# Kernel optimization log

Hardware: AMD Instinct MI355X
Metric: run time of the kernel (lower is better)

The kernel has to match this reference:

```python
import jax, jax.numpy as jnp
import numpy as np

B, S, D, H = 4, 2048, 1024, 16
HD = D // H  # 64

def setup_inputs() -> dict:
    key = jax.random.key(0)
    ks = jax.random.split(key, 6)
    scale = 1.0 / np.sqrt(D)
    return {
        "x": jax.random.normal(ks[0], (B, S, D), dtype=jnp.float32),
        "Wq": jax.random.normal(ks[1], (D, D), dtype=jnp.float32) * scale,
        "Wk": jax.random.normal(ks[2], (D, D), dtype=jnp.float32) * scale,
        "Wv": jax.random.normal(ks[3], (D, D), dtype=jnp.float32) * scale,
        "Wo": jax.random.normal(ks[4], (D, D), dtype=jnp.float32) * scale,
        "bo": jnp.zeros((D,), dtype=jnp.float32),
    }

def reference(x, Wq, Wk, Wv, Wo, bo):
    b, s, d = x.shape
    # projections (no bias for q/k/v, matching QKV_BIAS=False)
    q = (x @ Wq).reshape(b, s, H, HD).transpose(0, 2, 1, 3)  # [b,h,s,hd]
    k = (x @ Wk).reshape(b, s, H, HD).transpose(0, 2, 1, 3)
    v = (x @ Wv).reshape(b, s, H, HD).transpose(0, 2, 1, 3)
    scores = jnp.einsum('bhqd,bhkd->bhqk', q, k)  # [b,h,s,s]
    causal = jnp.tril(jnp.ones((s, s), dtype=bool))  # True where allowed
    scores = jnp.where(causal, scores, -jnp.inf)
    attn = jax.nn.softmax(scores / np.sqrt(HD), axis=-1)
    ctx = jnp.einsum('bhqk,bhkd->bhqd', attn, v)  # [b,h,s,hd]
    ctx = ctx.transpose(0, 2, 1, 3).reshape(b, s, d)
    return ctx @ Wo + bo
```

## Files before the change

kernel.cpp:

```cpp
#include <hip/hip_runtime.h>

#define BSZ 4
#define SEQ 2048
#define DIM 1024
#define NH  16
#define HD  64
#define QT  128
#define KT  64
#define PAD 72

typedef float v4f __attribute__((ext_vector_type(4)));
typedef short s8v __attribute__((ext_vector_type(8)));
typedef unsigned short u16;
typedef unsigned short u16x8 __attribute__((ext_vector_type(8)));
typedef unsigned short u16x4 __attribute__((ext_vector_type(4)));

__device__ __forceinline__ u16 f2bf(float f) {
  unsigned int u = __builtin_bit_cast(unsigned int, f);
  unsigned int r = u + 0x7fffu + ((u >> 16) & 1u);
  return (u16)(r >> 16);
}
__device__ __forceinline__ float bf2f(u16 h) {
  return __builtin_bit_cast(float, (unsigned int)h << 16);
}
__device__ __forceinline__ float fast_exp2(float x) {
#if __has_builtin(__builtin_amdgcn_exp2f)
  return __builtin_amdgcn_exp2f(x);
#else
  return exp2f(x);
#endif
}
__device__ __forceinline__ void gll16(const u16* g, u16* l) {
  __builtin_amdgcn_global_load_lds((const __attribute__((address_space(1))) void*)g,
                                   (__attribute__((address_space(3))) void*)l, 16, 0, 0);
}

__global__ __launch_bounds__(256) void cast_bf16_kernel(const float* __restrict__ x,
                                                        u16* __restrict__ o, int n4) {
  int i = blockIdx.x * 256 + threadIdx.x;
  if (i >= n4) return;
  v4f v = reinterpret_cast<const v4f*>(x)[i];
  u16x4 r;
  #pragma unroll
  for (int c = 0; c < 4; c++) r[c] = f2bf(v[c]);
  reinterpret_cast<u16x4*>(o)[i] = r;
}

__global__ __launch_bounds__(256) void transpose_cast_kernel(const float* __restrict__ W0,
                                                             const float* __restrict__ W1,
                                                             const float* __restrict__ W2,
                                                             const float* __restrict__ W3,
                                                             u16* __restrict__ out) {
  const float* W = blockIdx.z == 0 ? W0 : blockIdx.z == 1 ? W1 : blockIdx.z == 2 ? W2 : W3;
  u16* T = out + (size_t)blockIdx.z * DIM * DIM;
  __shared__ float tile[32][33];
  int tx = threadIdx.x & 31, ty = threadIdx.x >> 5;
  int bn = blockIdx.x * 32, bk = blockIdx.y * 32;
  #pragma unroll
  for (int r = 0; r < 4; r++) {
    int k = bk + ty + r * 8;
    tile[ty + r * 8][tx] = W[(size_t)k * DIM + bn + tx];
  }
  __syncthreads();
  #pragma unroll
  for (int r = 0; r < 4; r++) {
    int n = bn + ty + r * 8;
    T[(size_t)n * DIM + bk + tx] = f2bf(tile[tx][ty + r * 8]);
  }
}


#define GEMM_PROLOGUE()                                                          \
  const int t = threadIdx.x;                                                     \
  const int lane = t & 63, w = t >> 6;                                           \
  const int waveM = w >> 1, waveN = w & 1;                                       \
  const int quad = lane >> 4, l16 = lane & 15;                                   \
  __shared__ u16 Al[4096];                                                       \
  __shared__ u16 Bl[4096];                                                       \
  v4f acc[4][4];                                                                 \
  _Pragma("unroll") for (int i = 0; i < 4; i++)                                  \
    _Pragma("unroll") for (int j = 0; j < 4; j++)                                \
      acc[i][j] = (v4f){0.f, 0.f, 0.f, 0.f};                                     \
  const int sR = lane & 15, sC = lane >> 4;                                      \
  const u16* Ag0 = A  + (size_t)(m0 + (w * 2 + 0) * 16 + sR) * DIM + sC * 8;     \
  const u16* Ag1 = A  + (size_t)(m0 + (w * 2 + 1) * 16 + sR) * DIM + sC * 8;     \
  const u16* Bg0 = Bt + (size_t)(n0 + (w * 2 + 0) * 16 + sR) * DIM + sC * 8;     \
  const u16* Bg1 = Bt + (size_t)(n0 + (w * 2 + 1) * 16 + sR) * DIM + sC * 8;     \
  u16* Al0 = Al + (w * 2 + 0) * 512;                                             \
  u16* Al1 = Al + (w * 2 + 1) * 512;                                             \
  u16* Bl0 = Bl + (w * 2 + 0) * 512;                                             \
  u16* Bl1 = Bl + (w * 2 + 1) * 512;                                             \
  const int abase = waveM * 2048 + quad * 128 + l16 * 8;                         \
  const int bbase = waveN * 2048 + quad * 128 + l16 * 8;                         \
  for (int k0 = 0; k0 < DIM; k0 += 32) {                                         \
    __syncthreads();                                                             \
    gll16(Ag0 + k0, Al0); gll16(Ag1 + k0, Al1);                                  \
    gll16(Bg0 + k0, Bl0); gll16(Bg1 + k0, Bl1);                                  \
    __syncthreads();                                                             \
    s8v af[4], bfv[4];                                                           \
    _Pragma("unroll") for (int i = 0; i < 4; i++)                                \
      af[i] = *(const s8v*)(Al + abase + i * 512);                               \
    _Pragma("unroll") for (int j = 0; j < 4; j++)                                \
      bfv[j] = *(const s8v*)(Bl + bbase + j * 512);                              \
    _Pragma("unroll") for (int i = 0; i < 4; i++)                                \
      _Pragma("unroll") for (int j = 0; j < 4; j++)                              \
        acc[i][j] = __builtin_amdgcn_mfma_f32_16x16x32_bf16(af[i], bfv[j],       \
                                                            acc[i][j], 0, 0, 0); \
  }

__global__ __launch_bounds__(256) void gemm_qkv(const u16* __restrict__ A, const u16* __restrict__ Wt,
                                                u16* __restrict__ Qb, u16* __restrict__ Kb,
                                                u16* __restrict__ Vtg) {
  const int z = blockIdx.z;
  const u16* Bt = Wt + (size_t)z * DIM * DIM;
  const int n0 = blockIdx.x * 128, m0 = blockIdx.y * 128;
  GEMM_PROLOGUE()
  if (z == 2) {
    #pragma unroll
    for (int i = 0; i < 4; i++) {
      #pragma unroll
      for (int j = 0; j < 4; j++) {
        int gm0 = m0 + waveM * 64 + i * 16 + quad * 4;
        int gn = n0 + waveN * 64 + j * 16 + l16;
        int b = gm0 >> 11, s0 = gm0 & (SEQ - 1), hh = gn >> 6, d = gn & (HD - 1);
        u16x4 o;
        #pragma unroll
        for (int r = 0; r < 4; r++) o[r] = f2bf(acc[i][j][r]);
        *(u16x4*)(Vtg + ((size_t)(b * NH + hh) * HD + d) * SEQ + s0) = o;
      }
    }
  } else {
    u16* C = (z == 0) ? Qb : Kb;
    #pragma unroll
    for (int i = 0; i < 4; i++) {
      #pragma unroll
      for (int j = 0; j < 4; j++) {
        int gn = n0 + waveN * 64 + j * 16 + l16;
        #pragma unroll
        for (int r = 0; r < 4; r++) {
          int gm = m0 + waveM * 64 + i * 16 + quad * 4 + r;
          C[(size_t)gm * DIM + gn] = f2bf(acc[i][j][r]);
        }
      }
    }
  }
}

__global__ __launch_bounds__(256) void gemm_proj(const u16* __restrict__ A, const u16* __restrict__ Bt,
                                                 float* __restrict__ Cf, const float* __restrict__ bias) {
  const int n0 = blockIdx.x * 128, m0 = blockIdx.y * 128;
  GEMM_PROLOGUE()
  #pragma unroll
  for (int i = 0; i < 4; i++) {
    #pragma unroll
    for (int j = 0; j < 4; j++) {
      int gn = n0 + waveN * 64 + j * 16 + l16;
      float bv = bias[gn];
      #pragma unroll
      for (int r = 0; r < 4; r++) {
        int gm = m0 + waveM * 64 + i * 16 + quad * 4 + r;
        Cf[(size_t)gm * DIM + gn] = acc[i][j][r] + bv;
      }
    }
  }
}

__global__ __launch_bounds__(256, 2) void flash_attn_mfma(const u16* __restrict__ Qb,
                                                          const u16* __restrict__ Kb,
                                                          const u16* __restrict__ Vtg,
                                                          u16* __restrict__ Ob) {
  const int px = blockIdx.x, h = blockIdx.y, bb = blockIdx.z;
  const int t = threadIdx.x;
  const int lane = t & 63, w = t >> 6;
  const int quad = lane >> 4, l16 = lane & 15;

  __shared__ u16 QPs[QT * PAD];
  __shared__ u16 Ks[KT * PAD];
  __shared__ u16 Vs[HD * PAD];

  const size_t qkbase = (size_t)bb * SEQ * DIM + h * HD;
  const size_t vbase = ((size_t)bb * NH + h) * (size_t)HD * SEQ;

  const int vrow = t >> 2, scol = (t & 3) * 16;
  const int krow = ((vrow >> 5) + 2 * ((vrow >> 2) & 1)) * 16 + ((vrow >> 3) & 3) * 4 + (vrow & 3);

  for (int pass = 0; pass < 2; pass++) {
    const int qi = (pass == 0) ? px : (SEQ / QT - 1 - px);
    const int q0 = qi * QT;
    const int wq = q0 + w * 32;
    const int ntiles = 2 * qi + 2;

    __syncthreads();

    {
      const int r = t >> 1, c0 = (t & 1) * 32;
      const u16* src = Qb + qkbase + (size_t)(q0 + r) * DIM + c0;
      const float scq = 0.18033688011112042f;
      #pragma unroll
      for (int ch = 0; ch < 4; ch++) {
        u16x8 u = *(const u16x8*)(src + ch * 8);
        u16x8 o;
        #pragma unroll
        for (int j = 0; j < 8; j++) o[j] = f2bf(bf2f(u[j]) * scq);
        *(u16x8*)(QPs + r * PAD + c0 + ch * 8) = o;
      }
    }
    __syncthreads();

    s8v qf[2][2];
    #pragma unroll
    for (int ni = 0; ni < 2; ni++)
      #pragma unroll
      for (int kc = 0; kc < 2; kc++)
        qf[ni][kc] = *(const s8v*)(QPs + (w * 32 + ni * 16 + l16) * PAD + kc * 32 + quad * 8);

    u16x8 kr0, kr1, vr0, vr1;
    {
      const u16* kp = Kb + qkbase + (size_t)vrow * DIM + scol;
      kr0 = *(const u16x8*)kp; kr1 = *(const u16x8*)(kp + 8);
      const u16* vp = Vtg + vbase + (size_t)vrow * SEQ + scol;
      vr0 = *(const u16x8*)vp; vr1 = *(const u16x8*)(vp + 8);
    }

    float mrun[2] = {-1e30f, -1e30f}, lrun[2] = {0.f, 0.f};
    v4f O[4][2];
    #pragma unroll
    for (int di = 0; di < 4; di++)
      #pragma unroll
      for (int ni = 0; ni < 2; ni++) O[di][ni] = (v4f){0.f, 0.f, 0.f, 0.f};

    for (int it = 0; it < ntiles; ++it) {
      const int kv0 = it * KT;
      __syncthreads();
      *(u16x8*)(Ks + krow * PAD + scol) = kr0;
      *(u16x8*)(Ks + krow * PAD + scol + 8) = kr1;
      *(u16x8*)(Vs + vrow * PAD + scol) = vr0;
      *(u16x8*)(Vs + vrow * PAD + scol + 8) = vr1;
      __syncthreads();
      if (it + 1 < ntiles) {
        const int nkv = kv0 + KT;
        const u16* kp = Kb + qkbase + (size_t)(nkv + vrow) * DIM + scol;
        kr0 = *(const u16x8*)kp; kr1 = *(const u16x8*)(kp + 8);
        const u16* vp = Vtg + vbase + (size_t)vrow * SEQ + nkv + scol;
        vr0 = *(const u16x8*)vp; vr1 = *(const u16x8*)(vp + 8);
      }
      if (kv0 > wq + 31) continue;

      v4f sc[4][2];
      #pragma unroll
      for (int mi = 0; mi < 4; mi++)
        #pragma unroll
        for (int ni = 0; ni < 2; ni++) sc[mi][ni] = (v4f){0.f, 0.f, 0.f, 0.f};
      #pragma unroll
      for (int kc = 0; kc < 2; kc++) {
        #pragma unroll
        for (int mi = 0; mi < 4; mi++) {
          s8v kf = *(const s8v*)(Ks + (mi * 16 + l16) * PAD + kc * 32 + quad * 8);
          sc[mi][0] = __builtin_amdgcn_mfma_f32_16x16x32_bf16(kf, qf[0][kc], sc[mi][0], 0, 0, 0);
          sc[mi][1] = __builtin_amdgcn_mfma_f32_16x16x32_bf16(kf, qf[1][kc], sc[mi][1], 0, 0, 0);
        }
      }

      if (kv0 + KT > wq) {
        #pragma unroll
        for (int mi = 0; mi < 4; mi++) {
          const int kvb = kv0 + (mi & 1) * 32 + quad * 8 + (mi >> 1) * 4;
          #pragma unroll
          for (int ni = 0; ni < 2; ni++) {
            const int qg = wq + ni * 16 + l16;
            #pragma unroll
            for (int r = 0; r < 4; r++)
              if (kvb + r > qg) sc[mi][ni][r] = -1e30f;
          }
        }
      }

      float alpha[2];
      #pragma unroll
      for (int ni = 0; ni < 2; ni++) {
        float mx = -1e30f;
        #pragma unroll
        for (int mi = 0; mi < 4; mi++)
          #pragma unroll
          for (int r = 0; r < 4; r++) mx = fmaxf(mx, sc[mi][ni][r]);
        mx = fmaxf(mx, __shfl_xor(mx, 16, 64));
        mx = fmaxf(mx, __shfl_xor(mx, 32, 64));
        const float mnew = fmaxf(mrun[ni], mx);
        alpha[ni] = fast_exp2(mrun[ni] - mnew);
        mrun[ni] = mnew;
        float rsum = 0.f;
        #pragma unroll
        for (int mi = 0; mi < 4; mi++)
          #pragma unroll
          for (int r = 0; r < 4; r++) {
            float p = fast_exp2(sc[mi][ni][r] - mnew);
            sc[mi][ni][r] = p;
            rsum += p;
          }
        rsum += __shfl_xor(rsum, 16, 64);
        rsum += __shfl_xor(rsum, 32, 64);
        lrun[ni] = lrun[ni] * alpha[ni] + rsum;
      }
      #pragma unroll
      for (int di = 0; di < 4; di++)
        #pragma unroll
        for (int ni = 0; ni < 2; ni++)
          #pragma unroll
          for (int r = 0; r < 4; r++) O[di][ni][r] *= alpha[ni];

      s8v pf[2][2];
      #pragma unroll
      for (int ni = 0; ni < 2; ni++)
        #pragma unroll
        for (int kc = 0; kc < 2; kc++)
          #pragma unroll
          for (int j = 0; j < 8; j++)
            pf[ni][kc][j] = (short)f2bf(sc[kc + 2 * (j >> 2)][ni][j & 3]);

      #pragma unroll
      for (int kc = 0; kc < 2; kc++) {
        #pragma unroll
        for (int di = 0; di < 4; di++) {
          s8v vf = *(const s8v*)(Vs + (di * 16 + l16) * PAD + kc * 32 + quad * 8);
          O[di][0] = __builtin_amdgcn_mfma_f32_16x16x32_bf16(vf, pf[0][kc], O[di][0], 0, 0, 0);
          O[di][1] = __builtin_amdgcn_mfma_f32_16x16x32_bf16(vf, pf[1][kc], O[di][1], 0, 0, 0);
        }
      }
    }

    const float inv0 = 1.f / lrun[0], inv1 = 1.f / lrun[1];
    #pragma unroll
    for (int di = 0; di < 4; di++)
      #pragma unroll
      for (int ni = 0; ni < 2; ni++) {
        const float inv = ni ? inv1 : inv0;
        #pragma unroll
        for (int r = 0; r < 4; r++)
          QPs[(w * 32 + ni * 16 + l16) * PAD + di * 16 + quad * 4 + r] = f2bf(O[di][ni][r] * inv);
      }
    __syncthreads();
    {
      const int r = t >> 1, c0 = (t & 1) * 32;
      u16* dst = Ob + qkbase + (size_t)(q0 + r) * DIM + c0;
      #pragma unroll
      for (int ch = 0; ch < 4; ch++)
        *(u16x8*)(dst + ch * 8) = *(const u16x8*)(QPs + r * PAD + c0 + ch * 8);
    }
  }
}

extern "C" void kernel_launch(void* const* d_in, const int* in_sizes, int n_in,
                              void* d_out, int out_size, void* d_ws, size_t ws_size,
                              hipStream_t stream) {
  (void)in_sizes; (void)n_in; (void)out_size; (void)ws_size;
  const float* x  = (const float*)d_in[0];
  const float* Wq = (const float*)d_in[1];
  const float* Wk = (const float*)d_in[2];
  const float* Wv = (const float*)d_in[3];
  const float* Wo = (const float*)d_in[4];
  const float* bo = (const float*)d_in[5];
  float* out = (float*)d_out;

  char* ws = (char*)d_ws;
  const size_t MB = 1024ull * 1024ull;
  u16* Xb  = (u16*)(ws);
  u16* Wt  = (u16*)(ws + 16 * MB);
  u16* Qb  = (u16*)(ws + 24 * MB);
  u16* Kb  = (u16*)(ws + 40 * MB);
  u16* Vtg = (u16*)(ws + 56 * MB);
  u16* Cb  = (u16*)(ws + 72 * MB);

  const int NTOK = BSZ * SEQ;
  const int n4 = NTOK * DIM / 4;
  cast_bf16_kernel<<<(n4 + 255) / 256, 256, 0, stream>>>(x, Xb, n4);
  transpose_cast_kernel<<<dim3(32, 32, 4), 256, 0, stream>>>(Wq, Wk, Wv, Wo, Wt);

  gemm_qkv<<<dim3(DIM / 128, NTOK / 128, 3), 256, 0, stream>>>(Xb, Wt, Qb, Kb, Vtg);

  flash_attn_mfma<<<dim3(SEQ / QT / 2, NH, BSZ), 256, 0, stream>>>(Qb, Kb, Vtg, Cb);

  gemm_proj<<<dim3(DIM / 128, NTOK / 128), 256, 0, stream>>>(Cb, Wt + 3ull * DIM * DIM, out, bo);
}
```

Measured before the change: 316.7 us.

## Drop LDS staging in GEMMs and attention, fold Q scale into weights

The GEMMs now load MFMA operands directly from global memory (relying on L2/cache) instead of staging tiles through LDS with barriers. They also add an XCD-aware block swizzle and set launch_bounds occupancy to 2. Flash attention likewise reads K/V fragments straight from global memory, with no LDS or per-tile syncs, and swaps grid axes so heads are adjacent. Other changes: the softmax scale is folded into Wq at cast time, the O rescale is skipped when no alpha changed, and P is packed to bf16 with truncating perm instructions. The risk is higher global/L2 traffic and uncoalesced loads without LDS reuse, plus a small precision change from truncation.

```diff
diff --git a/kernel.cpp b/kernel.cpp
--- a/kernel.cpp
+++ b/kernel.cpp
@@ -14,14 +14,16 @@
 typedef unsigned short u16;
 typedef unsigned short u16x8 __attribute__((ext_vector_type(8)));
 typedef unsigned short u16x4 __attribute__((ext_vector_type(4)));
+typedef unsigned int u32;
+typedef unsigned int u32x4 __attribute__((ext_vector_type(4)));
 
 __device__ __forceinline__ u16 f2bf(float f) {
-  unsigned int u = __builtin_bit_cast(unsigned int, f);
-  unsigned int r = u + 0x7fffu + ((u >> 16) & 1u);
+  u32 u = __builtin_bit_cast(u32, f);
+  u32 r = u + 0x7fffu + ((u >> 16) & 1u);
   return (u16)(r >> 16);
 }
 __device__ __forceinline__ float bf2f(u16 h) {
-  return __builtin_bit_cast(float, (unsigned int)h << 16);
+  return __builtin_bit_cast(float, (u32)h << 16);
 }
 __device__ __forceinline__ float fast_exp2(float x) {
 #if __has_builtin(__builtin_amdgcn_exp2f)
@@ -30,9 +32,9 @@
   return exp2f(x);
 #endif
 }
-__device__ __forceinline__ void gll16(const u16* g, u16* l) {
-  __builtin_amdgcn_global_load_lds((const __attribute__((address_space(1))) void*)g,
-                                   (__attribute__((address_space(3))) void*)l, 16, 0, 0);
+__device__ __forceinline__ u32 pk2(float hi, float lo) {
+  return __builtin_amdgcn_perm(__builtin_bit_cast(u32, hi),
+                               __builtin_bit_cast(u32, lo), 0x07060302u);
 }
 
 __global__ __launch_bounds__(256) void cast_bf16_kernel(const float* __restrict__ x,
@@ -52,6 +54,7 @@
                                                              const float* __restrict__ W3,
                                                              u16* __restrict__ out) {
   const float* W = blockIdx.z == 0 ? W0 : blockIdx.z == 1 ? W1 : blockIdx.z == 2 ? W2 : W3;
+  const float scale = (blockIdx.z == 0) ? 0.18033688011112042f : 1.0f;
   u16* T = out + (size_t)blockIdx.z * DIM * DIM;
   __shared__ float tile[32][33];
   int tx = threadIdx.x & 31, ty = threadIdx.x >> 5;
@@ -65,56 +68,48 @@
   #pragma unroll
   for (int r = 0; r < 4; r++) {
     int n = bn + ty + r * 8;
-    T[(size_t)n * DIM + bk + tx] = f2bf(tile[tx][ty + r * 8]);
-  }
-}
-
-
-#define GEMM_PROLOGUE()                                                          \
+    T[(size_t)n * DIM + bk + tx] = f2bf(tile[tx][ty + r * 8] * scale);
+  }
+}
+
+
+#define GEMM_SETUP_AND_LOOP()                                                    \
+  const int flat = blockIdx.x + 8 * blockIdx.y;                                  \
+  const int xcd = flat & 7, slot = flat >> 3;                                    \
+  const int m0 = (xcd * 8 + (slot & 7)) * 128;                                   \
+  const int n0 = (slot >> 3) * 128;                                              \
   const int t = threadIdx.x;                                                     \
-  const int lane = t & 63, w = t >> 6;                                           \
-  const int waveM = w >> 1, waveN = w & 1;                                       \
+  const int lane = t & 63;                                                       \
+  const int waveM = (t >> 6) >> 1, waveN = (t >> 6) & 1;                         \
   const int quad = lane >> 4, l16 = lane & 15;                                   \
-  __shared__ u16 Al[4096];                                                       \
-  __shared__ u16 Bl[4096];                                                       \
   v4f acc[4][4];                                                                 \
   _Pragma("unroll") for (int i = 0; i < 4; i++)                                  \
     _Pragma("unroll") for (int j = 0; j < 4; j++)                                \
       acc[i][j] = (v4f){0.f, 0.f, 0.f, 0.f};                                     \
-  const int sR = lane & 15, sC = lane >> 4;                                      \
-  const u16* Ag0 = A  + (size_t)(m0 + (w * 2 + 0) * 16 + sR) * DIM + sC * 8;     \
-  const u16* Ag1 = A  + (size_t)(m0 + (w * 2 + 1) * 16 + sR) * DIM + sC * 8;     \
-  const u16* Bg0 = Bt + (size_t)(n0 + (w * 2 + 0) * 16 + sR) * DIM + sC * 8;     \
-  const u16* Bg1 = Bt + (size_t)(n0 + (w * 2 + 1) * 16 + sR) * DIM + sC * 8;     \
-  u16* Al0 = Al + (w * 2 + 0) * 512;                                             \
-  u16* Al1 = Al + (w * 2 + 1) * 512;                                             \
-  u16* Bl0 = Bl + (w * 2 + 0) * 512;                                             \
-  u16* Bl1 = Bl + (w * 2 + 1) * 512;                                             \
-  const int abase = waveM * 2048 + quad * 128 + l16 * 8;                         \
-  const int bbase = waveN * 2048 + quad * 128 + l16 * 8;                         \
-  for (int k0 = 0; k0 < DIM; k0 += 32) {                                         \
-    __syncthreads();                                                             \
-    gll16(Ag0 + k0, Al0); gll16(Ag1 + k0, Al1);                                  \
-    gll16(Bg0 + k0, Bl0); gll16(Bg1 + k0, Bl1);                                  \
-    __syncthreads();                                                             \
+  const u16* Ar[4];                                                              \
+  const u16* Br[4];                                                              \
+  _Pragma("unroll") for (int i = 0; i < 4; i++)                                  \
+    Ar[i] = A + (size_t)(m0 + waveM * 64 + i * 16 + l16) * DIM + quad * 8;       \
+  _Pragma("unroll") for (int j = 0; j < 4; j++)                                  \
+    Br[j] = Bt + (size_t)(n0 + waveN * 64 + j * 16 + l16) * DIM + quad * 8;      \
+  _Pragma("unroll 4") for (int k0 = 0; k0 < DIM; k0 += 32) {                     \
     s8v af[4], bfv[4];                                                           \
     _Pragma("unroll") for (int i = 0; i < 4; i++)                                \
-      af[i] = *(const s8v*)(Al + abase + i * 512);                               \
+      af[i] = *(const s8v*)(Ar[i] + k0);                                         \
     _Pragma("unroll") for (int j = 0; j < 4; j++)                                \
-      bfv[j] = *(const s8v*)(Bl + bbase + j * 512);                              \
+      bfv[j] = *(const s8v*)(Br[j] + k0);                                        \
     _Pragma("unroll") for (int i = 0; i < 4; i++)                                \
       _Pragma("unroll") for (int j = 0; j < 4; j++)                              \
         acc[i][j] = __builtin_amdgcn_mfma_f32_16x16x32_bf16(af[i], bfv[j],       \
                                                             acc[i][j], 0, 0, 0); \
   }
 
-__global__ __launch_bounds__(256) void gemm_qkv(const u16* __restrict__ A, const u16* __restrict__ Wt,
-                                                u16* __restrict__ Qb, u16* __restrict__ Kb,
-                                                u16* __restrict__ Vtg) {
+__global__ __launch_bounds__(256, 2) void gemm_qkv(const u16* __restrict__ A, const u16* __restrict__ Wt,
+                                                   u16* __restrict__ Qb, u16* __restrict__ Kb,
+                                                   u16* __restrict__ Vtg) {
   const int z = blockIdx.z;
   const u16* Bt = Wt + (size_t)z * DIM * DIM;
-  const int n0 = blockIdx.x * 128, m0 = blockIdx.y * 128;
-  GEMM_PROLOGUE()
+  GEMM_SETUP_AND_LOOP()
   if (z == 2) {
     #pragma unroll
     for (int i = 0; i < 4; i++) {
@@ -146,10 +141,9 @@
   }
 }
 
-__global__ __launch_bounds__(256) void gemm_proj(const u16* __restrict__ A, const u16* __restrict__ Bt,
-                                                 float* __restrict__ Cf, const float* __restrict__ bias) {
-  const int n0 = blockIdx.x * 128, m0 = blockIdx.y * 128;
-  GEMM_PROLOGUE()
+__global__ __launch_bounds__(256, 2) void gemm_proj(const u16* __restrict__ A, const u16* __restrict__ Bt,
+                                                    float* __restrict__ Cf, const float* __restrict__ bias) {
+  GEMM_SETUP_AND_LOOP()
   #pragma unroll
   for (int i = 0; i < 4; i++) {
     #pragma unroll
@@ -169,58 +163,40 @@
                                                           const u16* __restrict__ Kb,
                                                           const u16* __restrict__ Vtg,
                                                           u16* __restrict__ Ob) {
-  const int px = blockIdx.x, h = blockIdx.y, bb = blockIdx.z;
+  const int h = blockIdx.x, px = blockIdx.y, bb = blockIdx.z;
   const int t = threadIdx.x;
   const int lane = t & 63, w = t >> 6;
   const int quad = lane >> 4, l16 = lane & 15;
 
   __shared__ u16 QPs[QT * PAD];
-  __shared__ u16 Ks[KT * PAD];
-  __shared__ u16 Vs[HD * PAD];
 
   const size_t qkbase = (size_t)bb * SEQ * DIM + h * HD;
   const size_t vbase = ((size_t)bb * NH + h) * (size_t)HD * SEQ;
 
-  const int vrow = t >> 2, scol = (t & 3) * 16;
-  const int krow = ((vrow >> 5) + 2 * ((vrow >> 2) & 1)) * 16 + ((vrow >> 3) & 3) * 4 + (vrow & 3);
+  const u16* Kp[4];
+  #pragma unroll
+  for (int mi = 0; mi < 4; mi++) {
+    const int rowoff = (mi & 1) * 32 + (mi >> 1) * 4 + (l16 >> 2) * 8 + (l16 & 3);
+    Kp[mi] = Kb + qkbase + (size_t)rowoff * DIM + quad * 8;
+  }
+  const u16* Vp[4];
+  #pragma unroll
+  for (int di = 0; di < 4; di++)
+    Vp[di] = Vtg + vbase + (size_t)(di * 16 + l16) * SEQ + quad * 8;
 
   for (int pass = 0; pass < 2; pass++) {
     const int qi = (pass == 0) ? px : (SEQ / QT - 1 - px);
     const int q0 = qi * QT;
     const int wq = q0 + w * 32;
-    const int ntiles = 2 * qi + 2;
-
-    __syncthreads();
-
-    {
-      const int r = t >> 1, c0 = (t & 1) * 32;
-      const u16* src = Qb + qkbase + (size_t)(q0 + r) * DIM + c0;
-      const float scq = 0.18033688011112042f;
-      #pragma unroll
-      for (int ch = 0; ch < 4; ch++) {
-        u16x8 u = *(const u16x8*)(src + ch * 8);
-        u16x8 o;
-        #pragma unroll
-        for (int j = 0; j < 8; j++) o[j] = f2bf(bf2f(u[j]) * scq);
-        *(u16x8*)(QPs + r * PAD + c0 + ch * 8) = o;
-      }
-    }
-    __syncthreads();
+    const int itmax = (wq + 31) >> 6;
 
     s8v qf[2][2];
     #pragma unroll
     for (int ni = 0; ni < 2; ni++)
       #pragma unroll
       for (int kc = 0; kc < 2; kc++)
-        qf[ni][kc] = *(const s8v*)(QPs + (w * 32 + ni * 16 + l16) * PAD + kc * 32 + quad * 8);
-
-    u16x8 kr0, kr1, vr0, vr1;
-    {
-      const u16* kp = Kb + qkbase + (size_t)vrow * DIM + scol;
-      kr0 = *(const u16x8*)kp; kr1 = *(const u16x8*)(kp + 8);
-      const u16* vp = Vtg + vbase + (size_t)vrow * SEQ + scol;
-      vr0 = *(const u16x8*)vp; vr1 = *(const u16x8*)(vp + 8);
-    }
+        qf[ni][kc] = *(const s8v*)(Qb + qkbase +
+            (size_t)(q0 + w * 32 + ni * 16 + l16) * DIM + kc * 32 + quad * 8);
 
     float mrun[2] = {-1e30f, -1e30f}, lrun[2] = {0.f, 0.f};
     v4f O[4][2];
@@ -229,22 +205,20 @@
       #pragma unroll
       for (int ni = 0; ni < 2; ni++) O[di][ni] = (v4f){0.f, 0.f, 0.f, 0.f};
 
-    for (int it = 0; it < ntiles; ++it) {
+    for (int it = 0; it <= itmax; ++it) {
       const int kv0 = it * KT;
-      __syncthreads();
-      *(u16x8*)(Ks + krow * PAD + scol) = kr0;
-      *(u16x8*)(Ks + krow * PAD + scol + 8) = kr1;
-      *(u16x8*)(Vs + vrow * PAD + scol) = vr0;
-      *(u16x8*)(Vs + vrow * PAD + scol + 8) = vr1;
-      __syncthreads();
-      if (it + 1 < ntiles) {
-        const int nkv = kv0 + KT;
-        const u16* kp = Kb + qkbase + (size_t)(nkv + vrow) * DIM + scol;
-        kr0 = *(const u16x8*)kp; kr1 = *(const u16x8*)(kp + 8);
-        const u16* vp = Vtg + vbase + (size_t)vrow * SEQ + nkv + scol;
-        vr0 = *(const u16x8*)vp; vr1 = *(const u16x8*)(vp + 8);
-      }
-      if (kv0 > wq + 31) continue;
+
+      s8v kf[4][2], vf[4][2];
+      #pragma unroll
+      for (int mi = 0; mi < 4; mi++) {
+        kf[mi][0] = *(const s8v*)(Kp[mi] + (size_t)kv0 * DIM);
+        kf[mi][1] = *(const s8v*)(Kp[mi] + (size_t)kv0 * DIM + 32);
+      }
+      #pragma unroll
+      for (int di = 0; di < 4; di++) {
+        vf[di][0] = *(const s8v*)(Vp[di] + kv0);
+        vf[di][1] = *(const s8v*)(Vp[di] + kv0 + 32);
+      }
 
       v4f sc[4][2];
       #pragma unroll
@@ -252,14 +226,12 @@
         #pragma unroll
         for (int ni = 0; ni < 2; ni++) sc[mi][ni] = (v4f){0.f, 0.f, 0.f, 0.f};
       #pragma unroll
-      for (int kc = 0; kc < 2; kc++) {
+      for (int kc = 0; kc < 2; kc++)
         #pragma unroll
         for (int mi = 0; mi < 4; mi++) {
-          s8v kf = *(const s8v*)(Ks + (mi * 16 + l16) * PAD + kc * 32 + quad * 8);
-          sc[mi][0] = __builtin_amdgcn_mfma_f32_16x16x32_bf16(kf, qf[0][kc], sc[mi][0], 0, 0, 0);
-          sc[mi][1] = __builtin_amdgcn_mfma_f32_16x16x32_bf16(kf, qf[1][kc], sc[mi][1], 0, 0, 0);
-        }
-      }
+          sc[mi][0] = __builtin_amdgcn_mfma_f32_16x16x32_bf16(kf[mi][kc], qf[0][kc], sc[mi][0], 0, 0, 0);
+          sc[mi][1] = __builtin_amdgcn_mfma_f32_16x16x32_bf16(kf[mi][kc], qf[1][kc], sc[mi][1], 0, 0, 0);
+        }
 
       if (kv0 + KT > wq) {
         #pragma unroll
@@ -301,31 +273,35 @@
         rsum += __shfl_xor(rsum, 32, 64);
         lrun[ni] = lrun[ni] * alpha[ni] + rsum;
       }
-      #pragma unroll
-      for (int di = 0; di < 4; di++)
-        #pragma unroll
-        for (int ni = 0; ni < 2; ni++)
+      if (__any((alpha[0] != 1.0f) | (alpha[1] != 1.0f))) {
+        #pragma unroll
+        for (int di = 0; di < 4; di++)
           #pragma unroll
-          for (int r = 0; r < 4; r++) O[di][ni][r] *= alpha[ni];
+          for (int ni = 0; ni < 2; ni++)
+            #pragma unroll
+            for (int r = 0; r < 4; r++) O[di][ni][r] *= alpha[ni];
+      }
 
       s8v pf[2][2];
       #pragma unroll
       for (int ni = 0; ni < 2; ni++)
         #pragma unroll
-        for (int kc = 0; kc < 2; kc++)
-          #pragma unroll
-          for (int j = 0; j < 8; j++)
-            pf[ni][kc][j] = (short)f2bf(sc[kc + 2 * (j >> 2)][ni][j & 3]);
-
-      #pragma unroll
-      for (int kc = 0; kc < 2; kc++) {
+        for (int kc = 0; kc < 2; kc++) {
+          u32x4 pw;
+          pw[0] = pk2(sc[kc][ni][1], sc[kc][ni][0]);
+          pw[1] = pk2(sc[kc][ni][3], sc[kc][ni][2]);
+          pw[2] = pk2(sc[kc + 2][ni][1], sc[kc + 2][ni][0]);
+          pw[3] = pk2(sc[kc + 2][ni][3], sc[kc + 2][ni][2]);
+          pf[ni][kc] = __builtin_bit_cast(s8v, pw);
+        }
+
+      #pragma unroll
+      for (int kc = 0; kc < 2; kc++)
         #pragma unroll
         for (int di = 0; di < 4; di++) {
-          s8v vf = *(const s8v*)(Vs + (di * 16 + l16) * PAD + kc * 32 + quad * 8);
-          O[di][0] = __builtin_amdgcn_mfma_f32_16x16x32_bf16(vf, pf[0][kc], O[di][0], 0, 0, 0);
-          O[di][1] = __builtin_amdgcn_mfma_f32_16x16x32_bf16(vf, pf[1][kc], O[di][1], 0, 0, 0);
-        }
-      }
+          O[di][0] = __builtin_amdgcn_mfma_f32_16x16x32_bf16(vf[di][kc], pf[0][kc], O[di][0], 0, 0, 0);
+          O[di][1] = __builtin_amdgcn_mfma_f32_16x16x32_bf16(vf[di][kc], pf[1][kc], O[di][1], 0, 0, 0);
+        }
     }
 
     const float inv0 = 1.f / lrun[0], inv1 = 1.f / lrun[1];
@@ -346,6 +322,7 @@
       for (int ch = 0; ch < 4; ch++)
         *(u16x8*)(dst + ch * 8) = *(const u16x8*)(QPs + r * PAD + c0 + ch * 8);
     }
+    __syncthreads();
   }
 }
 
@@ -377,7 +354,7 @@
 
   gemm_qkv<<<dim3(DIM / 128, NTOK / 128, 3), 256, 0, stream>>>(Xb, Wt, Qb, Kb, Vtg);
 
-  flash_attn_mfma<<<dim3(SEQ / QT / 2, NH, BSZ), 256, 0, stream>>>(Qb, Kb, Vtg, Cb);
+  flash_attn_mfma<<<dim3(NH, SEQ / QT / 2, BSZ), 256, 0, stream>>>(Qb, Kb, Vtg, Cb);
 
   gemm_proj<<<dim3(DIM / 128, NTOK / 128), 256, 0, stream>>>(Cb, Wt + 3ull * DIM * DIM, out, bo);
 }
```

New measurement: 464.2 us. 46.6% more time.

## Double-buffer GEMM loads, remap tiles per XCD, fold Q scale into Wq

Applied to the files above, without the earlier changes.

The QKV and output-projection GEMMs switch to per-wave double-buffered LDS staging that uses vmcnt waits in place of two block barriers per k-step. Block indices are remapped so neighbouring M tiles land on the same XCD for cache reuse, and the launch bounds now allow two blocks per CU. The softmax scale for Q is folded into Wq during the weight transpose, which removes the per-element rescale in the attention kernel. Attention grid axes are swapped (heads first) and occupancy is raised to three blocks. Risks: Q now takes two bf16 roundings in a different order, LDS use grows to 64KB per GEMM block, and per-wave buffers rely on each wave reading only its own loads.

```diff
diff --git a/kernel.cpp b/kernel.cpp
--- a/kernel.cpp
+++ b/kernel.cpp
@@ -14,14 +14,15 @@
 typedef unsigned short u16;
 typedef unsigned short u16x8 __attribute__((ext_vector_type(8)));
 typedef unsigned short u16x4 __attribute__((ext_vector_type(4)));
+typedef unsigned int u32;
 
 __device__ __forceinline__ u16 f2bf(float f) {
-  unsigned int u = __builtin_bit_cast(unsigned int, f);
-  unsigned int r = u + 0x7fffu + ((u >> 16) & 1u);
+  u32 u = __builtin_bit_cast(u32, f);
+  u32 r = u + 0x7fffu + ((u >> 16) & 1u);
   return (u16)(r >> 16);
 }
 __device__ __forceinline__ float bf2f(u16 h) {
-  return __builtin_bit_cast(float, (unsigned int)h << 16);
+  return __builtin_bit_cast(float, (u32)h << 16);
 }
 __device__ __forceinline__ float fast_exp2(float x) {
 #if __has_builtin(__builtin_amdgcn_exp2f)
@@ -34,6 +35,8 @@
   __builtin_amdgcn_global_load_lds((const __attribute__((address_space(1))) void*)g,
                                    (__attribute__((address_space(3))) void*)l, 16, 0, 0);
 }
+#define WAITCNT_VM8 0xF78
+#define WAITCNT_VM0 0xF70
 
 __global__ __launch_bounds__(256) void cast_bf16_kernel(const float* __restrict__ x,
                                                         u16* __restrict__ o, int n4) {
@@ -52,6 +55,7 @@
                                                              const float* __restrict__ W3,
                                                              u16* __restrict__ out) {
   const float* W = blockIdx.z == 0 ? W0 : blockIdx.z == 1 ? W1 : blockIdx.z == 2 ? W2 : W3;
+  const float scale = (blockIdx.z == 0) ? 0.18033688011112042f : 1.0f;
   u16* T = out + (size_t)blockIdx.z * DIM * DIM;
   __shared__ float tile[32][33];
   int tx = threadIdx.x & 31, ty = threadIdx.x >> 5;
@@ -65,56 +69,68 @@
   #pragma unroll
   for (int r = 0; r < 4; r++) {
     int n = bn + ty + r * 8;
-    T[(size_t)n * DIM + bk + tx] = f2bf(tile[tx][ty + r * 8]);
-  }
-}
-
-
-#define GEMM_PROLOGUE()                                                          \
-  const int t = threadIdx.x;                                                     \
-  const int lane = t & 63, w = t >> 6;                                           \
-  const int waveM = w >> 1, waveN = w & 1;                                       \
-  const int quad = lane >> 4, l16 = lane & 15;                                   \
-  __shared__ u16 Al[4096];                                                       \
-  __shared__ u16 Bl[4096];                                                       \
-  v4f acc[4][4];                                                                 \
-  _Pragma("unroll") for (int i = 0; i < 4; i++)                                  \
-    _Pragma("unroll") for (int j = 0; j < 4; j++)                                \
-      acc[i][j] = (v4f){0.f, 0.f, 0.f, 0.f};                                     \
-  const int sR = lane & 15, sC = lane >> 4;                                      \
-  const u16* Ag0 = A  + (size_t)(m0 + (w * 2 + 0) * 16 + sR) * DIM + sC * 8;     \
-  const u16* Ag1 = A  + (size_t)(m0 + (w * 2 + 1) * 16 + sR) * DIM + sC * 8;     \
-  const u16* Bg0 = Bt + (size_t)(n0 + (w * 2 + 0) * 16 + sR) * DIM + sC * 8;     \
-  const u16* Bg1 = Bt + (size_t)(n0 + (w * 2 + 1) * 16 + sR) * DIM + sC * 8;     \
-  u16* Al0 = Al + (w * 2 + 0) * 512;                                             \
-  u16* Al1 = Al + (w * 2 + 1) * 512;                                             \
-  u16* Bl0 = Bl + (w * 2 + 0) * 512;                                             \
-  u16* Bl1 = Bl + (w * 2 + 1) * 512;                                             \
-  const int abase = waveM * 2048 + quad * 128 + l16 * 8;                         \
-  const int bbase = waveN * 2048 + quad * 128 + l16 * 8;                         \
-  for (int k0 = 0; k0 < DIM; k0 += 32) {                                         \
-    __syncthreads();                                                             \
-    gll16(Ag0 + k0, Al0); gll16(Ag1 + k0, Al1);                                  \
-    gll16(Bg0 + k0, Bl0); gll16(Bg1 + k0, Bl1);                                  \
-    __syncthreads();                                                             \
-    s8v af[4], bfv[4];                                                           \
-    _Pragma("unroll") for (int i = 0; i < 4; i++)                                \
-      af[i] = *(const s8v*)(Al + abase + i * 512);                               \
-    _Pragma("unroll") for (int j = 0; j < 4; j++)                                \
-      bfv[j] = *(const s8v*)(Bl + bbase + j * 512);                              \
-    _Pragma("unroll") for (int i = 0; i < 4; i++)                                \
-      _Pragma("unroll") for (int j = 0; j < 4; j++)                              \
-        acc[i][j] = __builtin_amdgcn_mfma_f32_16x16x32_bf16(af[i], bfv[j],       \
-                                                            acc[i][j], 0, 0, 0); \
-  }
-
-__global__ __launch_bounds__(256) void gemm_qkv(const u16* __restrict__ A, const u16* __restrict__ Wt,
-                                                u16* __restrict__ Qb, u16* __restrict__ Kb,
-                                                u16* __restrict__ Vtg) {
+    T[(size_t)n * DIM + bk + tx] = f2bf(tile[tx][ty + r * 8] * scale);
+  }
+}
+
+
+#define GEMM_HALF(rdofs, wrofs, knext)                                            \
+  { if ((knext) < DIM) {                                                          \
+      _Pragma("unroll") for (int i = 0; i < 4; i++)                               \
+        gll16(Ag[i] + (knext), Aw + (wrofs) + i * 512);                           \
+      _Pragma("unroll") for (int j = 0; j < 4; j++)                               \
+        gll16(Bg[j] + (knext), Bw + (wrofs) + j * 512);                           \
+      __builtin_amdgcn_s_waitcnt(WAITCNT_VM8);                                    \
+    } else {                                                                      \
+      __builtin_amdgcn_s_waitcnt(WAITCNT_VM0);                                    \
+    }                                                                             \
+    s8v af[4], bfv[4];                                                            \
+    _Pragma("unroll") for (int i = 0; i < 4; i++)                                 \
+      af[i] = *(const s8v*)(Aw + (rdofs) + i * 512 + quad * 128 + l16 * 8);       \
+    _Pragma("unroll") for (int j = 0; j < 4; j++)                                 \
+      bfv[j] = *(const s8v*)(Bw + (rdofs) + j * 512 + quad * 128 + l16 * 8);      \
+    _Pragma("unroll") for (int i = 0; i < 4; i++)                                 \
+      _Pragma("unroll") for (int j = 0; j < 4; j++)                               \
+        acc[i][j] = __builtin_amdgcn_mfma_f32_16x16x32_bf16(af[i], bfv[j],        \
+                                                            acc[i][j], 0, 0, 0); }
+
+#define GEMM_SETUP_AND_LOOP()                                                     \
+  const int flat = blockIdx.x + 8 * blockIdx.y;                                   \
+  const int xcd = flat & 7, slot = flat >> 3;                                     \
+  const int m0 = (xcd * 8 + (slot & 7)) * 128;                                    \
+  const int n0 = (slot >> 3) * 128;                                               \
+  const int t = threadIdx.x;                                                      \
+  const int lane = t & 63, w = t >> 6;                                            \
+  const int waveM = w >> 1, waveN = w & 1;                                        \
+  const int quad = lane >> 4, l16 = lane & 15;                                    \
+  __shared__ u16 Al[16384];                                                       \
+  __shared__ u16 Bl[16384];                                                       \
+  u16* Aw = Al + w * 4096;                                                        \
+  u16* Bw = Bl + w * 4096;                                                        \
+  v4f acc[4][4];                                                                  \
+  _Pragma("unroll") for (int i = 0; i < 4; i++)                                   \
+    _Pragma("unroll") for (int j = 0; j < 4; j++)                                 \
+      acc[i][j] = (v4f){0.f, 0.f, 0.f, 0.f};                                      \
+  const int sR = lane & 15, sC = lane >> 4;                                       \
+  const u16* Ag[4];                                                               \
+  const u16* Bg[4];                                                               \
+  _Pragma("unroll") for (int i = 0; i < 4; i++)                                   \
+    Ag[i] = A + (size_t)(m0 + waveM * 64 + i * 16 + sR) * DIM + sC * 8;           \
+  _Pragma("unroll") for (int j = 0; j < 4; j++)                                   \
+    Bg[j] = Bt + (size_t)(n0 + waveN * 64 + j * 16 + sR) * DIM + sC * 8;          \
+  _Pragma("unroll") for (int i = 0; i < 4; i++) gll16(Ag[i], Aw + i * 512);       \
+  _Pragma("unroll") for (int j = 0; j < 4; j++) gll16(Bg[j], Bw + j * 512);       \
+  for (int k0 = 0; k0 < DIM; k0 += 64) {                                          \
+    GEMM_HALF(0, 2048, k0 + 32)                                                   \
+    GEMM_HALF(2048, 0, k0 + 64)                                                   \
+  }
+
+__global__ __launch_bounds__(256, 2) void gemm_qkv(const u16* __restrict__ A, const u16* __restrict__ Wt,
+                                                   u16* __restrict__ Qb, u16* __restrict__ Kb,
+                                                   u16* __restrict__ Vtg) {
   const int z = blockIdx.z;
   const u16* Bt = Wt + (size_t)z * DIM * DIM;
-  const int n0 = blockIdx.x * 128, m0 = blockIdx.y * 128;
-  GEMM_PROLOGUE()
+  GEMM_SETUP_AND_LOOP()
   if (z == 2) {
     #pragma unroll
     for (int i = 0; i < 4; i++) {
@@ -146,10 +162,9 @@
   }
 }
 
-__global__ __launch_bounds__(256) void gemm_proj(const u16* __restrict__ A, const u16* __restrict__ Bt,
-                                                 float* __restrict__ Cf, const float* __restrict__ bias) {
-  const int n0 = blockIdx.x * 128, m0 = blockIdx.y * 128;
-  GEMM_PROLOGUE()
+__global__ __launch_bounds__(256, 2) void gemm_proj(const u16* __restrict__ A, const u16* __restrict__ Bt,
+                                                    float* __restrict__ Cf, const float* __restrict__ bias) {
+  GEMM_SETUP_AND_LOOP()
   #pragma unroll
   for (int i = 0; i < 4; i++) {
     #pragma unroll
@@ -165,11 +180,11 @@
   }
 }
 
-__global__ __launch_bounds__(256, 2) void flash_attn_mfma(const u16* __restrict__ Qb,
+__global__ __launch_bounds__(256, 3) void flash_attn_mfma(const u16* __restrict__ Qb,
                                                           const u16* __restrict__ Kb,
                                                           const u16* __restrict__ Vtg,
                                                           u16* __restrict__ Ob) {
-  const int px = blockIdx.x, h = blockIdx.y, bb = blockIdx.z;
+  const int h = blockIdx.x, px = blockIdx.y, bb = blockIdx.z;
   const int t = threadIdx.x;
   const int lane = t & 63, w = t >> 6;
   const int quad = lane >> 4, l16 = lane & 15;
@@ -195,15 +210,9 @@
     {
       const int r = t >> 1, c0 = (t & 1) * 32;
       const u16* src = Qb + qkbase + (size_t)(q0 + r) * DIM + c0;
-      const float scq = 0.18033688011112042f;
-      #pragma unroll
-      for (int ch = 0; ch < 4; ch++) {
-        u16x8 u = *(const u16x8*)(src + ch * 8);
-        u16x8 o;
-        #pragma unroll
-        for (int j = 0; j < 8; j++) o[j] = f2bf(bf2f(u[j]) * scq);
-        *(u16x8*)(QPs + r * PAD + c0 + ch * 8) = o;
-      }
+      #pragma unroll
+      for (int ch = 0; ch < 4; ch++)
+        *(u16x8*)(QPs + r * PAD + c0 + ch * 8) = *(const u16x8*)(src + ch * 8);
     }
     __syncthreads();
 
@@ -377,7 +386,7 @@
 
   gemm_qkv<<<dim3(DIM / 128, NTOK / 128, 3), 256, 0, stream>>>(Xb, Wt, Qb, Kb, Vtg);
 
-  flash_attn_mfma<<<dim3(SEQ / QT / 2, NH, BSZ), 256, 0, stream>>>(Qb, Kb, Vtg, Cb);
+  flash_attn_mfma<<<dim3(NH, SEQ / QT / 2, BSZ), 256, 0, stream>>>(Qb, Kb, Vtg, Cb);
 
   gemm_proj<<<dim3(DIM / 128, NTOK / 128), 256, 0, stream>>>(Cb, Wt + 3ull * DIM * DIM, out, bo);
 }
```

Result: slower. 404.5 us (+27.7%).
